# Optimization experiments

Hardware: AMD Instinct MI355X
Metric: run time of the kernel (lower is better)

The kernel has to match this reference:

```python
import jax, jax.numpy as jnp
import numpy as np

N_EMBED = 1024
N_HEADS = 16
CTX = 2048
B, T = 4, 2048
HD = N_EMBED // N_HEADS


def setup_inputs() -> dict:
    key = jax.random.key(0)
    ks = jax.random.split(key, 5)
    scale = 1.0 / np.sqrt(N_EMBED)
    return {
        "x": jax.random.normal(ks[0], (B, T, N_EMBED), dtype=jnp.float32),
        "wq": jax.random.normal(ks[1], (N_EMBED, N_EMBED), dtype=jnp.float32) * scale,
        "wk": jax.random.normal(ks[2], (N_EMBED, N_EMBED), dtype=jnp.float32) * scale,
        "wv": jax.random.normal(ks[3], (N_EMBED, N_EMBED), dtype=jnp.float32) * scale,
        "wo": jax.random.normal(ks[4], (N_EMBED, N_EMBED), dtype=jnp.float32) * scale,
    }


def reference(x, wq, wk, wv, wo):
    b, t, c = x.shape
    # nn.Linear applies x @ W.T ; split heads -> [B, H, T, hd]
    def proj(w):
        return jnp.einsum("btc,dc->btd", x, w).reshape(b, t, N_HEADS, HD).transpose(0, 2, 1, 3)
    q, k, v = proj(wq), proj(wk), proj(wv)
    scores = jnp.einsum("bhqd,bhkd->bhqk", q, k) * (HD ** -0.5)
    causal = jnp.tril(jnp.ones((t, t), dtype=bool))
    scores = jnp.where(causal[None, None, :, :], scores, -jnp.inf)
    a = jax.nn.softmax(scores, axis=-1)
    o = jnp.einsum("bhqk,bhkd->bhqd", a, v)  # [B,H,T,hd]
    o = o.transpose(0, 2, 1, 3).reshape(b, t, c)
    return jnp.einsum("btc,dc->btd", o, wo)
```

## Files before the change

kernel.cpp:

```cpp
#include <hip/hip_runtime.h>
#include <stdint.h>


typedef __attribute__((ext_vector_type(8))) short bf16x8;
typedef __attribute__((ext_vector_type(4))) float f32x4;
typedef __attribute__((ext_vector_type(16))) float f32x16;
typedef unsigned short us;
typedef unsigned int u32;

#define LOG2E 1.4426950408889634f

#define GL2LDS16(g, l)                                                          \
  __builtin_amdgcn_global_load_lds(                                             \
      (const __attribute__((address_space(1))) unsigned int*)(g),               \
      (__attribute__((address_space(3))) unsigned int*)(l), 16, 0, 0)

__device__ inline us f2bf(float f) {
  union { float f; unsigned int u; } v; v.f = f;
  unsigned int u = v.u;
  u += 0x7FFFu + ((u >> 16) & 1u);
  return (us)(u >> 16);
}

__global__ void cast_all(const float* __restrict__ x,
                         const float* __restrict__ w0, const float* __restrict__ w1,
                         const float* __restrict__ w2, const float* __restrict__ w3,
                         us* __restrict__ xb, us* __restrict__ wbuf) {
  int i = (blockIdx.x * blockDim.x + threadIdx.x) * 8;
  const float* src;
  us* dst;
  float sc = 1.0f;
  if (i < (8 << 20)) {
    src = x + i; dst = xb + i;
  } else {
    int j = i - (8 << 20);
    int seg = j >> 20;
    int off = j & ((1 << 20) - 1);
    const float* w = (seg == 0) ? w0 : (seg == 1) ? w1 : (seg == 2) ? w2 : w3;
    if (seg == 0) sc = 0.125f * LOG2E;
    src = w + off; dst = wbuf + j;
  }
  float4 a = *reinterpret_cast<const float4*>(src);
  float4 b = *reinterpret_cast<const float4*>(src + 4);
  union { us u[8]; uint4 v; } o;
  o.u[0] = f2bf(a.x * sc); o.u[1] = f2bf(a.y * sc);
  o.u[2] = f2bf(a.z * sc); o.u[3] = f2bf(a.w * sc);
  o.u[4] = f2bf(b.x * sc); o.u[5] = f2bf(b.y * sc);
  o.u[6] = f2bf(b.z * sc); o.u[7] = f2bf(b.w * sc);
  *reinterpret_cast<uint4*>(dst) = o.v;
}

__global__ __launch_bounds__(256, 3) void gemm_qkv(
    const us* __restrict__ A, const us* __restrict__ Bw,
    us* __restrict__ QKV, us* __restrict__ Vt) {
  const int K = 1024, N = 3072;
  __shared__ __align__(16) us Al[128 * 64];
  __shared__ __align__(16) us Bl[128 * 64];
  const int tid = threadIdx.x;
  const int lane = tid & 63;
  const int w = tid >> 6;
  const int quad = lane >> 4;
  const int l16 = lane & 15;
  const int bid = blockIdx.x;
  const int xcd = bid & 7;
  const int idx = bid >> 3;
  const int mt = xcd * 8 + idx / 24;
  const int nt = idx % 24;
  const int m0 = mt * 128;
  const int n0 = nt * 128;
  const int wm = w >> 1, wn = w & 1;
  const int srow_base = w * 8 + (lane >> 3);
  const int sunit = lane & 7;
  f32x4 acc[4][4] = {};

  for (int k0 = 0; k0 < K; k0 += 64) {
    __syncthreads();
#pragma unroll
    for (int it = 0; it < 4; ++it) {
      int row = it * 32 + srow_base;
      int gu = sunit ^ (row & 7);
      int base = __builtin_amdgcn_readfirstlane((it * 256 + w * 64) * 8);
      GL2LDS16(A + (size_t)(m0 + row) * K + k0 + gu * 8, &Al[base]);
      GL2LDS16(Bw + (size_t)(n0 + row) * K + k0 + gu * 8, &Bl[base]);
    }
    __syncthreads();
#pragma unroll
    for (int kk = 0; kk < 2; ++kk) {
      bf16x8 af[4], bfr[4];
#pragma unroll
      for (int mi = 0; mi < 4; ++mi) {
        int row = wm * 64 + mi * 16 + l16;
        af[mi] = *reinterpret_cast<const bf16x8*>(
            &Al[row * 64 + (((kk * 4 + quad) ^ (row & 7)) * 8)]);
      }
#pragma unroll
      for (int ni = 0; ni < 4; ++ni) {
        int row = wn * 64 + ni * 16 + l16;
        bfr[ni] = *reinterpret_cast<const bf16x8*>(
            &Bl[row * 64 + (((kk * 4 + quad) ^ (row & 7)) * 8)]);
      }
#pragma unroll
      for (int mi = 0; mi < 4; ++mi)
#pragma unroll
        for (int ni = 0; ni < 4; ++ni)
          acc[mi][ni] = __builtin_amdgcn_mfma_f32_16x16x32_bf16(af[mi], bfr[ni], acc[mi][ni], 0, 0, 0);
    }
  }

  if (n0 < 2048) {
#pragma unroll
    for (int mi = 0; mi < 4; ++mi)
#pragma unroll
      for (int ni = 0; ni < 4; ++ni)
#pragma unroll
        for (int r = 0; r < 4; ++r) {
          int row = m0 + wm * 64 + mi * 16 + quad * 4 + r;
          int col = n0 + wn * 64 + ni * 16 + l16;
          QKV[(size_t)row * N + col] = f2bf(acc[mi][ni][r]);
        }
  } else {
    const int bI = m0 >> 11;
    const int tbase = m0 & 2047;
#pragma unroll
    for (int mi = 0; mi < 4; ++mi)
#pragma unroll
      for (int ni = 0; ni < 4; ++ni)
#pragma unroll
        for (int r = 0; r < 4; ++r) {
          int krow = tbase + wm * 64 + mi * 16 + quad * 4 + r;
          int col = n0 + wn * 64 + ni * 16 + l16;
          int hh = (col - 2048) >> 6;
          int d = col & 63;
          Vt[((size_t)((bI * 16 + hh) * 64 + d)) * 2048 + krow] = f2bf(acc[mi][ni][r]);
        }
  }
}

__global__ __launch_bounds__(256, 2) void gemm_out(
    const us* __restrict__ A, const us* __restrict__ Bw,
    float* __restrict__ Cv, int M, int N, int K) {
  __shared__ __align__(16) us Al[128 * 64];
  __shared__ __align__(16) us Bl[128 * 64];
  const int tid = threadIdx.x;
  const int lane = tid & 63;
  const int w = tid >> 6;
  const int quad = lane >> 4;
  const int l16 = lane & 15;
  const int m0 = blockIdx.y * 128;
  const int n0 = blockIdx.x * 128;
  const int wm = w >> 1, wn = w & 1;
  const int srow_base = w * 8 + (lane >> 3);
  const int sunit = lane & 7;
  f32x4 acc[4][4] = {};

  for (int k0 = 0; k0 < K; k0 += 64) {
    __syncthreads();
#pragma unroll
    for (int it = 0; it < 4; ++it) {
      int row = it * 32 + srow_base;
      int gu = sunit ^ (row & 7);
      int base = __builtin_amdgcn_readfirstlane((it * 256 + w * 64) * 8);
      GL2LDS16(A + (size_t)(m0 + row) * K + k0 + gu * 8, &Al[base]);
      GL2LDS16(Bw + (size_t)(n0 + row) * K + k0 + gu * 8, &Bl[base]);
    }
    __syncthreads();
#pragma unroll
    for (int kk = 0; kk < 2; ++kk) {
      bf16x8 af[4], bfr[4];
#pragma unroll
      for (int mi = 0; mi < 4; ++mi) {
        int row = wm * 64 + mi * 16 + l16;
        af[mi] = *reinterpret_cast<const bf16x8*>(
            &Al[row * 64 + (((kk * 4 + quad) ^ (row & 7)) * 8)]);
      }
#pragma unroll
      for (int ni = 0; ni < 4; ++ni) {
        int row = wn * 64 + ni * 16 + l16;
        bfr[ni] = *reinterpret_cast<const bf16x8*>(
            &Bl[row * 64 + (((kk * 4 + quad) ^ (row & 7)) * 8)]);
      }
#pragma unroll
      for (int mi = 0; mi < 4; ++mi)
#pragma unroll
        for (int ni = 0; ni < 4; ++ni)
          acc[mi][ni] = __builtin_amdgcn_mfma_f32_16x16x32_bf16(af[mi], bfr[ni], acc[mi][ni], 0, 0, 0);
    }
  }

#pragma unroll
  for (int mi = 0; mi < 4; ++mi)
#pragma unroll
    for (int ni = 0; ni < 4; ++ni)
#pragma unroll
      for (int r = 0; r < 4; ++r) {
        int row = m0 + wm * 64 + mi * 16 + quad * 4 + r;
        int col = n0 + wn * 64 + ni * 16 + l16;
        Cv[(size_t)row * N + col] = acc[mi][ni][r];
      }
}

__global__ __launch_bounds__(256, 3) void attn(
    const us* __restrict__ QKV, const us* __restrict__ Vt,
    us* __restrict__ O) {
  __shared__ __align__(16) us Kb[2][64 * 64];
  __shared__ __align__(16) us Vb[2][64 * 64];
  __shared__ float Ls[4][32];
  const int bid = blockIdx.x;
  const int j16 = bid >> 6;
  const int grp = j16 >> 2, pos = j16 & 3;
  const int qt = (grp == 0) ? 15 - pos : (grp == 1) ? pos
               : (grp == 2) ? 11 - pos : 4 + pos;
  const int bh = bid & 63;
  const int b = bh >> 4, h = bh & 15;
  const int q0 = qt * 128;
  const int tid = threadIdx.x, lane = tid & 63, w = tid >> 6;
  const int l31 = lane & 31, hi = lane >> 5;
  const size_t rowbase = (size_t)b * 2048;
  const int qcol = h * 64;
  const int kcol = 1024 + h * 64;
  const int qw = q0 + w * 32;
  const int nT = 2 * qt + 2;

  const int mr = (l31 & 7) ^ ((l31 >> 3) & 3);

  bf16x8 qf[4];
#pragma unroll
  for (int ds = 0; ds < 4; ++ds)
    qf[ds] = *reinterpret_cast<const bf16x8*>(
        &QKV[(rowbase + qw + l31) * 3072 + qcol + ds * 16 + hi * 8]);

  f32x16 oacc[2] = {};
  float psum = 0.f;

  const int rr8 = w * 8 + (lane >> 3);
  const int ms = (rr8 & 7) ^ ((rr8 >> 3) & 3);
  const int uu = lane & 7;
  const int gu = uu ^ ms;

  auto stage = [&](int kt, int buf) {
#pragma unroll
    for (int c = 0; c < 2; ++c) {
      int row = c * 32 + rr8;
      int base = __builtin_amdgcn_readfirstlane((c * 32 + w * 8) * 64);
      GL2LDS16(QKV + (rowbase + kt * 64 + row) * 3072 + kcol + gu * 8,
               &Kb[buf][base]);
      GL2LDS16(Vt + ((size_t)(bh * 64 + row)) * 2048 + kt * 64 + gu * 8,
               &Vb[buf][base]);
    }
  };

  stage(0, 0);

  for (int kt = 0; kt < nT; ++kt) {
    asm volatile("s_waitcnt vmcnt(0)" ::: "memory");
    asm volatile("s_barrier" ::: "memory");
    if (kt + 1 < nT) stage(kt + 1, (kt + 1) & 1);
    const us* Kl = &Kb[kt & 1][0];
    const us* Vl = &Vb[kt & 1][0];

    const int kdiff = qw + 31 - kt * 64;
    if (kdiff < 0) continue;
    const int tmax = (kdiff >= 32) ? 2 : 1;
    const bool do_mask = (kt * 64 + 63) > qw;

#pragma unroll
    for (int t = 0; t < 2; ++t) {
      if (t < tmax) {
        f32x16 s = {};
#pragma unroll
        for (int ds = 0; ds < 4; ++ds) {
          int row = t * 32 + l31;
          bf16x8 kf = *reinterpret_cast<const bf16x8*>(
              &Kl[row * 64 + (((ds * 2 + hi) ^ mr) * 8)]);
          s = __builtin_amdgcn_mfma_f32_32x32x16_bf16(kf, qf[ds], s, 0, 0, 0);
        }

        float p[16];
        if (do_mask) {
#pragma unroll
          for (int r = 0; r < 16; ++r) {
            float e = __builtin_amdgcn_exp2f(s[r]);
            int kg = kt * 64 + t * 32 + (r & 3) + ((r >> 2) << 3) + hi * 4;
            p[r] = (kg <= qw + l31) ? e : 0.f;
            psum += p[r];
          }
        } else {
#pragma unroll
          for (int r = 0; r < 16; ++r) {
            p[r] = __builtin_amdgcn_exp2f(s[r]);
            psum += p[r];
          }
        }

        u32 pk[4][2];
#pragma unroll
        for (int bb = 0; bb < 4; ++bb)
#pragma unroll
          for (int w2 = 0; w2 < 2; ++w2)
            asm("v_cvt_pk_bf16_f32 %0, %1, %2"
                : "=v"(pk[bb][w2])
                : "v"(p[4 * bb + 2 * w2]), "v"(p[4 * bb + 2 * w2 + 1]));

#pragma unroll
        for (int s2 = 0; s2 < 2; ++s2) {
          u32 pa[4];
#pragma unroll
          for (int w2 = 0; w2 < 2; ++w2) {
            u32 a = pk[2 * s2][w2];
            u32 c = pk[2 * s2 + 1][w2];
            asm volatile("v_permlane32_swap_b32 %0, %1" : "+v"(a), "+v"(c));
            pa[w2] = a;
            pa[2 + w2] = c;
          }
          union { u32 u[4]; bf16x8 v; } pu;
          pu.u[0] = pa[0]; pu.u[1] = pa[1]; pu.u[2] = pa[2]; pu.u[3] = pa[3];
          bf16x8 paf = pu.v;
          int ks = t * 2 + s2;
#pragma unroll
          for (int dt = 0; dt < 2; ++dt) {
            int row = dt * 32 + l31;
            bf16x8 vf = *reinterpret_cast<const bf16x8*>(
                &Vl[row * 64 + (((ks * 2 + hi) ^ mr) * 8)]);
            oacc[dt] = __builtin_amdgcn_mfma_f32_32x32x16_bf16(paf, vf, oacc[dt], 0, 0, 0);
          }
        }
      }
    }
  }

  {
    float a = psum, c = psum;
    asm volatile("v_permlane32_swap_b32 %0, %1" : "+v"(a), "+v"(c));
    float invl = 1.0f / (a + c);
    if (!hi) Ls[w][l31] = invl;
    asm volatile("s_waitcnt lgkmcnt(0)" ::: "memory");
  }
  float inv[16];
#pragma unroll
  for (int r = 0; r < 16; ++r)
    inv[r] = Ls[w][(r & 3) + ((r >> 2) << 3) + hi * 4];
#pragma unroll
  for (int dt = 0; dt < 2; ++dt)
#pragma unroll
    for (int r = 0; r < 16; ++r) {
      int qg = qw + (r & 3) + ((r >> 2) << 3) + hi * 4;
      O[(rowbase + qg) * 1024 + qcol + dt * 32 + l31] = f2bf(oacc[dt][r] * inv[r]);
    }
}

extern "C" void kernel_launch(void* const* d_in, const int* in_sizes, int n_in,
                              void* d_out, int out_size, void* d_ws, size_t ws_size,
                              hipStream_t stream) {
  const float* x = (const float*)d_in[0];
  const float* wq = (const float*)d_in[1];
  const float* wk = (const float*)d_in[2];
  const float* wv = (const float*)d_in[3];
  const float* wo = (const float*)d_in[4];

  const int BT = 8192, E = 1024;
  const size_t NX = (size_t)BT * E;
  const size_t NW = (size_t)E * E;

  us* xb = (us*)d_ws;
  us* wbuf = xb + NX;
  us* QKV = wbuf + 4 * NW;
  us* VtB = QKV + (size_t)BT * 3 * E;
  us* Ob = xb;

  cast_all<<<(int)((NX + 4 * NW) / 8 / 256), 256, 0, stream>>>(x, wq, wk, wv, wo, xb, wbuf);

  gemm_qkv<<<1536, 256, 0, stream>>>(xb, wbuf, QKV, VtB);
  attn<<<1024, 256, 0, stream>>>(QKV, VtB, Ob);
  gemm_out<<<dim3(8, 64), 256, 0, stream>>>(Ob, wbuf + 3 * NW, (float*)d_out, BT, E, E);
}
```

Baseline: 230.1 us.

## Process two 32-row query tiles per wave in attention, halving block size

The attention kernel now runs 2 waves per block instead of 4, and each wave handles two 32-row query slices (rows w*32 and 64+w*32). Each K/V fragment read from LDS then feeds two MFMAs, halving LDS read traffic per unit of compute, and the staging loop is rewritten for 128 threads. The cost is roughly doubled accumulator and Q register use, lower occupancy (launch bounds 128,2), and fewer waves per block to hide the barrier and global-to-LDS loads.

```diff
diff --git a/kernel.cpp b/kernel.cpp
--- a/kernel.cpp
+++ b/kernel.cpp
@@ -199,12 +199,12 @@
       }
 }
 
-__global__ __launch_bounds__(256, 3) void attn(
+__global__ __launch_bounds__(128, 2) void attn(
     const us* __restrict__ QKV, const us* __restrict__ Vt,
     us* __restrict__ O) {
   __shared__ __align__(16) us Kb[2][64 * 64];
   __shared__ __align__(16) us Vb[2][64 * 64];
-  __shared__ float Ls[4][32];
+  __shared__ float Ls[2][2][32];
   const int bid = blockIdx.x;
   const int j16 = bid >> 6;
   const int grp = j16 >> 2, pos = j16 & 3;
@@ -218,30 +218,33 @@
   const size_t rowbase = (size_t)b * 2048;
   const int qcol = h * 64;
   const int kcol = 1024 + h * 64;
-  const int qw = q0 + w * 32;
+  const int qw0 = q0 + w * 32;
+  const int qw1 = q0 + 64 + w * 32;
   const int nT = 2 * qt + 2;
 
   const int mr = (l31 & 7) ^ ((l31 >> 3) & 3);
 
-  bf16x8 qf[4];
-#pragma unroll
-  for (int ds = 0; ds < 4; ++ds)
-    qf[ds] = *reinterpret_cast<const bf16x8*>(
-        &QKV[(rowbase + qw + l31) * 3072 + qcol + ds * 16 + hi * 8]);
-
-  f32x16 oacc[2] = {};
-  float psum = 0.f;
+  bf16x8 qf0[4], qf1[4];
+#pragma unroll
+  for (int ds = 0; ds < 4; ++ds) {
+    qf0[ds] = *reinterpret_cast<const bf16x8*>(
+        &QKV[(rowbase + qw0 + l31) * 3072 + qcol + ds * 16 + hi * 8]);
+    qf1[ds] = *reinterpret_cast<const bf16x8*>(
+        &QKV[(rowbase + qw1 + l31) * 3072 + qcol + ds * 16 + hi * 8]);
+  }
+
+  f32x16 oacc0[2] = {}, oacc1[2] = {};
+  float psum0 = 0.f, psum1 = 0.f;
 
   const int rr8 = w * 8 + (lane >> 3);
-  const int ms = (rr8 & 7) ^ ((rr8 >> 3) & 3);
   const int uu = lane & 7;
-  const int gu = uu ^ ms;
 
   auto stage = [&](int kt, int buf) {
 #pragma unroll
-    for (int c = 0; c < 2; ++c) {
-      int row = c * 32 + rr8;
-      int base = __builtin_amdgcn_readfirstlane((c * 32 + w * 8) * 64);
+    for (int c = 0; c < 4; ++c) {
+      int row = c * 16 + rr8;
+      int gu = uu ^ ((rr8 & 7) ^ ((2 * c + (rr8 >> 3)) & 3));
+      int base = __builtin_amdgcn_readfirstlane((c * 128 + w * 64) * 8);
       GL2LDS16(QKV + (rowbase + kt * 64 + row) * 3072 + kcol + gu * 8,
                &Kb[buf][base]);
       GL2LDS16(Vt + ((size_t)(bh * 64 + row)) * 2048 + kt * 64 + gu * 8,
@@ -257,94 +260,121 @@
     if (kt + 1 < nT) stage(kt + 1, (kt + 1) & 1);
     const us* Kl = &Kb[kt & 1][0];
     const us* Vl = &Vb[kt & 1][0];
-
-    const int kdiff = qw + 31 - kt * 64;
-    if (kdiff < 0) continue;
-    const int tmax = (kdiff >= 32) ? 2 : 1;
-    const bool do_mask = (kt * 64 + 63) > qw;
+    const int kb = kt * 64;
+
+    const int kd1 = qw1 + 31 - kb;
+    if (kd1 < 0) continue;
+    const int kd0 = qw0 + 31 - kb;
+    const int tmax0 = (kd0 < 0) ? 0 : ((kd0 >= 32) ? 2 : 1);
+    const int tmax1 = (kd1 >= 32) ? 2 : 1;
+    const bool mk0 = (kb + 63) > qw0;
+    const bool mk1 = (kb + 63) > qw1;
+
+    u32 pa0[4][4], pa1[4][4];
+
+#define PACK(S, DOMASK, QW, PSUM, PA, T)                                       \
+    {                                                                          \
+      float p[16];                                                             \
+      if (DOMASK) {                                                            \
+        _Pragma("unroll")                                                      \
+        for (int r = 0; r < 16; ++r) {                                         \
+          float e = __builtin_amdgcn_exp2f(S[r]);                              \
+          int kg = kb + (T) * 32 + (r & 3) + ((r >> 2) << 3) + hi * 4;         \
+          p[r] = (kg <= (QW) + l31) ? e : 0.f;                                 \
+          PSUM += p[r];                                                        \
+        }                                                                      \
+      } else {                                                                 \
+        _Pragma("unroll")                                                      \
+        for (int r = 0; r < 16; ++r) { p[r] = __builtin_amdgcn_exp2f(S[r]); PSUM += p[r]; } \
+      }                                                                        \
+      u32 pk[4][2];                                                            \
+      _Pragma("unroll")                                                        \
+      for (int bb = 0; bb < 4; ++bb)                                           \
+        _Pragma("unroll")                                                      \
+        for (int w2 = 0; w2 < 2; ++w2)                                         \
+          asm("v_cvt_pk_bf16_f32 %0, %1, %2"                                   \
+              : "=v"(pk[bb][w2])                                               \
+              : "v"(p[4 * bb + 2 * w2]), "v"(p[4 * bb + 2 * w2 + 1]));         \
+      _Pragma("unroll")                                                        \
+      for (int s2 = 0; s2 < 2; ++s2)                                           \
+        _Pragma("unroll")                                                      \
+        for (int w2 = 0; w2 < 2; ++w2) {                                       \
+          u32 a_ = pk[2 * s2][w2];                                             \
+          u32 c_ = pk[2 * s2 + 1][w2];                                         \
+          asm volatile("v_permlane32_swap_b32 %0, %1" : "+v"(a_), "+v"(c_));   \
+          PA[(T) * 2 + s2][w2] = a_;                                           \
+          PA[(T) * 2 + s2][2 + w2] = c_;                                       \
+        }                                                                      \
+    }
 
 #pragma unroll
     for (int t = 0; t < 2; ++t) {
-      if (t < tmax) {
-        f32x16 s = {};
+      if (t < tmax1) {
+        const bool a0 = t < tmax0;
+        f32x16 s0 = {}, s1 = {};
 #pragma unroll
         for (int ds = 0; ds < 4; ++ds) {
           int row = t * 32 + l31;
           bf16x8 kf = *reinterpret_cast<const bf16x8*>(
               &Kl[row * 64 + (((ds * 2 + hi) ^ mr) * 8)]);
-          s = __builtin_amdgcn_mfma_f32_32x32x16_bf16(kf, qf[ds], s, 0, 0, 0);
+          s1 = __builtin_amdgcn_mfma_f32_32x32x16_bf16(kf, qf1[ds], s1, 0, 0, 0);
+          if (a0)
+            s0 = __builtin_amdgcn_mfma_f32_32x32x16_bf16(kf, qf0[ds], s0, 0, 0, 0);
         }
-
-        float p[16];
-        if (do_mask) {
-#pragma unroll
-          for (int r = 0; r < 16; ++r) {
-            float e = __builtin_amdgcn_exp2f(s[r]);
-            int kg = kt * 64 + t * 32 + (r & 3) + ((r >> 2) << 3) + hi * 4;
-            p[r] = (kg <= qw + l31) ? e : 0.f;
-            psum += p[r];
-          }
-        } else {
-#pragma unroll
-          for (int r = 0; r < 16; ++r) {
-            p[r] = __builtin_amdgcn_exp2f(s[r]);
-            psum += p[r];
-          }
+        PACK(s1, mk1, qw1, psum1, pa1, t)
+        if (a0) PACK(s0, mk0, qw0, psum0, pa0, t)
+      }
+    }
+#undef PACK
+
+    const int ks1 = tmax1 * 2, ks0 = tmax0 * 2;
+#pragma unroll
+    for (int ks = 0; ks < 4; ++ks) {
+      if (ks < ks1) {
+        union { u32 u[4]; bf16x8 v; } p1u;
+        p1u.u[0] = pa1[ks][0]; p1u.u[1] = pa1[ks][1];
+        p1u.u[2] = pa1[ks][2]; p1u.u[3] = pa1[ks][3];
+        union { u32 u[4]; bf16x8 v; } p0u;
+        p0u.u[0] = pa0[ks][0]; p0u.u[1] = pa0[ks][1];
+        p0u.u[2] = pa0[ks][2]; p0u.u[3] = pa0[ks][3];
+#pragma unroll
+        for (int dt = 0; dt < 2; ++dt) {
+          int row = dt * 32 + l31;
+          bf16x8 vf = *reinterpret_cast<const bf16x8*>(
+              &Vl[row * 64 + (((ks * 2 + hi) ^ mr) * 8)]);
+          oacc1[dt] = __builtin_amdgcn_mfma_f32_32x32x16_bf16(p1u.v, vf, oacc1[dt], 0, 0, 0);
+          if (ks < ks0)
+            oacc0[dt] = __builtin_amdgcn_mfma_f32_32x32x16_bf16(p0u.v, vf, oacc0[dt], 0, 0, 0);
         }
-
-        u32 pk[4][2];
-#pragma unroll
-        for (int bb = 0; bb < 4; ++bb)
-#pragma unroll
-          for (int w2 = 0; w2 < 2; ++w2)
-            asm("v_cvt_pk_bf16_f32 %0, %1, %2"
-                : "=v"(pk[bb][w2])
-                : "v"(p[4 * bb + 2 * w2]), "v"(p[4 * bb + 2 * w2 + 1]));
-
-#pragma unroll
-        for (int s2 = 0; s2 < 2; ++s2) {
-          u32 pa[4];
-#pragma unroll
-          for (int w2 = 0; w2 < 2; ++w2) {
-            u32 a = pk[2 * s2][w2];
-            u32 c = pk[2 * s2 + 1][w2];
-            asm volatile("v_permlane32_swap_b32 %0, %1" : "+v"(a), "+v"(c));
-            pa[w2] = a;
-            pa[2 + w2] = c;
-          }
-          union { u32 u[4]; bf16x8 v; } pu;
-          pu.u[0] = pa[0]; pu.u[1] = pa[1]; pu.u[2] = pa[2]; pu.u[3] = pa[3];
-          bf16x8 paf = pu.v;
-          int ks = t * 2 + s2;
-#pragma unroll
-          for (int dt = 0; dt < 2; ++dt) {
-            int row = dt * 32 + l31;
-            bf16x8 vf = *reinterpret_cast<const bf16x8*>(
-                &Vl[row * 64 + (((ks * 2 + hi) ^ mr) * 8)]);
-            oacc[dt] = __builtin_amdgcn_mfma_f32_32x32x16_bf16(paf, vf, oacc[dt], 0, 0, 0);
-          }
-        }
       }
     }
   }
 
   {
-    float a = psum, c = psum;
-    asm volatile("v_permlane32_swap_b32 %0, %1" : "+v"(a), "+v"(c));
-    float invl = 1.0f / (a + c);
-    if (!hi) Ls[w][l31] = invl;
+    float a0 = psum0, c0 = psum0;
+    asm volatile("v_permlane32_swap_b32 %0, %1" : "+v"(a0), "+v"(c0));
+    float a1 = psum1, c1 = psum1;
+    asm volatile("v_permlane32_swap_b32 %0, %1" : "+v"(a1), "+v"(c1));
+    if (!hi) {
+      Ls[w][0][l31] = 1.0f / (a0 + c0);
+      Ls[w][1][l31] = 1.0f / (a1 + c1);
+    }
     asm volatile("s_waitcnt lgkmcnt(0)" ::: "memory");
   }
-  float inv[16];
-#pragma unroll
-  for (int r = 0; r < 16; ++r)
-    inv[r] = Ls[w][(r & 3) + ((r >> 2) << 3) + hi * 4];
+  float inv0[16], inv1[16];
+#pragma unroll
+  for (int r = 0; r < 16; ++r) {
+    int rq = (r & 3) + ((r >> 2) << 3) + hi * 4;
+    inv0[r] = Ls[w][0][rq];
+    inv1[r] = Ls[w][1][rq];
+  }
 #pragma unroll
   for (int dt = 0; dt < 2; ++dt)
 #pragma unroll
     for (int r = 0; r < 16; ++r) {
-      int qg = qw + (r & 3) + ((r >> 2) << 3) + hi * 4;
-      O[(rowbase + qg) * 1024 + qcol + dt * 32 + l31] = f2bf(oacc[dt][r] * inv[r]);
+      int rq = (r & 3) + ((r >> 2) << 3) + hi * 4;
+      O[(rowbase + qw0 + rq) * 1024 + qcol + dt * 32 + l31] = f2bf(oacc0[dt][r] * inv0[r]);
+      O[(rowbase + qw1 + rq) * 1024 + qcol + dt * 32 + l31] = f2bf(oacc1[dt][r] * inv1[r]);
     }
 }
 
@@ -370,6 +400,6 @@
   cast_all<<<(int)((NX + 4 * NW) / 8 / 256), 256, 0, stream>>>(x, wq, wk, wv, wo, xb, wbuf);
 
   gemm_qkv<<<1536, 256, 0, stream>>>(xb, wbuf, QKV, VtB);
-  attn<<<1024, 256, 0, stream>>>(QKV, VtB, Ob);
+  attn<<<1024, 128, 0, stream>>>(QKV, VtB, Ob);
   gemm_out<<<dim3(8, 64), 256, 0, stream>>>(Ob, wbuf + 3 * NW, (float*)d_out, BT, E, E);
 }
```

New measurement: 272.8 us. +18.6%, slower.
